# Optimization experiments

Measured on AMD Instinct MI355X. Metric: run time of the kernel, lower is better.

Reference implementation:

```python
import jax, jax.numpy as jnp
import numpy as np
from itertools import permutations
from math import factorial

N_MODES = 6
BATCH = 32768

# Clements mesh mode pairs for 6 modes: alternating odd/even layers, 15 MZIs total.
def clements_mode_list(n=6):
    pairs = []
    for layer in range(n):
        start = 0 if layer % 2 == 0 else 1
        for m in range(start, n - 1, 2):
            pairs.append((m, m + 1))
    return pairs

CLEMENTS_MODES = clements_mode_list(6)            # 15 pairs
ANSATZ_MODES = [(0, 1), (2, 3), (4, 5), (1, 2), (3, 4)] * 2  # 10 pairs (0-indexed)

IN_CONFIG = [1, 1, 1, 0, 0, 0]
OUT_CONFIGS = [list(c) for c in [
    [1,1,1,0,0,0],[1,1,0,1,0,0],[1,1,0,0,1,0],[1,1,0,0,0,1],[1,0,1,1,0,0],
    [1,0,1,0,1,0],[1,0,1,0,0,1],[1,0,0,1,1,0],[1,0,0,1,0,1],[1,0,0,0,1,1],
    [0,1,1,1,0,0],[0,1,1,0,1,0],[0,1,1,0,0,1],[0,1,0,1,1,0],[0,1,0,1,0,1],
    [0,1,0,0,1,1],[0,0,1,1,1,0],[0,0,1,1,0,1],[0,0,1,0,1,1],[0,0,0,1,1,1]]]

def _expand(config):  # occupation list -> repeated mode indices
    idx = []
    for m, c in enumerate(config):
        idx += [m] * int(c)
    return idx

IN_IDX = np.array(_expand(IN_CONFIG))                       # [3]
OUT_IDX = np.array([_expand(c) for c in OUT_CONFIGS])       # [20, 3]
N_PH = IN_IDX.shape[0]                                      # 3 photons
PERMS = list(permutations(range(N_PH)))                     # 6 perms of S_3
# boson-sampling normalization: sqrt(prod(in!) * prod(out!)) per output config (all 1 here)
NORM = np.array([np.sqrt(np.prod([factorial(int(v)) for v in IN_CONFIG]) *
                         np.prod([factorial(int(v)) for v in c])) for c in OUT_CONFIGS],
                dtype=np.float32)


def calc_unitary(modes, theta, phi):
    """Chain of MZI 2x2 rotations embedded in a 6x6 identity (Clements convention)."""
    U = jnp.eye(N_MODES, dtype=jnp.complex64)
    for k, (m, n) in enumerate(modes):
        ct = jnp.cos(theta[k]).astype(jnp.complex64)
        st = jnp.sin(theta[k]).astype(jnp.complex64)
        ep = jnp.exp(1j * phi[k].astype(jnp.complex64))
        T = jnp.eye(N_MODES, dtype=jnp.complex64)
        T = T.at[m, m].set(ep * ct).at[m, n].set(-st)
        T = T.at[n, m].set(ep * st).at[n, n].set(ct)
        U = T @ U
    return U


def permanent3(M):  # M: [..., 3, 3] complex -> [...] permanent over S_3
    acc = jnp.zeros(M.shape[:-2], dtype=M.dtype)
    for p in PERMS:
        acc = acc + M[..., 0, p[0]] * M[..., 1, p[1]] * M[..., 2, p[2]]
    return acc


def setup_inputs() -> dict:
    key = jax.random.key(0)
    ks = jax.random.split(key, 7)
    return {
        "x": jax.random.normal(ks[0], (BATCH, 12), dtype=jnp.float32),
        "params": jax.random.normal(ks[1], (30,), dtype=jnp.float32),
        "output_phase": jax.random.normal(ks[2], (6,), dtype=jnp.float32),
        "param_phi": jax.random.normal(ks[3], (4,), dtype=jnp.float32),
        "param_theta": jax.random.normal(ks[4], (4,), dtype=jnp.float32),
        "input_k": jax.random.normal(ks[5], (12,), dtype=jnp.float32),
        "input_b": jax.random.normal(ks[6], (12,), dtype=jnp.float32),
    }


def reference(x, params, output_phase, param_phi, param_theta, input_k, input_b):
    B = x.shape[0]
    # Static 6x6 interferometer: phi = params[0:15], theta = params[15:30]
    start = calc_unitary(CLEMENTS_MODES, params[15:30], params[0:15])
    start = jnp.diag(jnp.exp(1j * output_phase.astype(jnp.complex64))) @ start

    # Data-reuploading ansatz angles, [B, 10] each
    xs = x * input_k + input_b
    phi = jnp.concatenate([xs[:, 0:3], jnp.broadcast_to(param_phi[0:2], (B, 2)),
                           xs[:, 6:9], jnp.broadcast_to(param_phi[2:4], (B, 2))], axis=1)
    theta = jnp.concatenate([xs[:, 3:6], jnp.broadcast_to(param_theta[0:2], (B, 2)),
                             xs[:, 9:12], jnp.broadcast_to(param_theta[2:4], (B, 2))], axis=1)

    U_ans = jax.vmap(lambda t, p: calc_unitary(ANSATZ_MODES, t, p))(theta, phi)  # [B,6,6]
    U_final = U_ans @ start                                                      # [B,6,6]

    # Boson-sampling amplitudes: permanent of [out rows, in cols] submatrix
    sub = U_final[:, OUT_IDX[:, :, None], IN_IDX[None, None, :]]  # [B, 20, 3, 3]
    amps = permanent3(sub) / jnp.asarray(NORM)                    # [B, 20] complex

    # F.normalize(p=2, dim=1, eps=1e-12) on complex vectors
    norm = jnp.sqrt(jnp.sum(jnp.abs(amps) ** 2, axis=1, keepdims=True))
    amps = amps / jnp.maximum(norm, 1e-12)
    return jnp.abs(amps)
```

## Files before the change

### kernel.cpp

```cpp
#include <hip/hip_runtime.h>
#include <math.h>


__global__ __launch_bounds__(64) void bqnn_kernel(
    const float* __restrict__ x,
    const float* __restrict__ params,
    const float* __restrict__ output_phase,
    const float* __restrict__ param_phi,
    const float* __restrict__ param_theta,
    const float* __restrict__ input_k,
    const float* __restrict__ input_b,
    float* __restrict__ out,
    int B)
{
    __shared__ float sc[88];
    int lane = threadIdx.x;
    int b = blockIdx.x * 64 + lane;
    int bl = (b < B) ? b : (B - 1);

    const float4* xp = reinterpret_cast<const float4*>(x + (size_t)bl * 12);
    float4 a0 = xp[0], a1 = xp[1], a2 = xp[2];

    if (lane < 44) {
        float arg;
        if      (lane < 15) arg = params[15 + lane];
        else if (lane < 30) arg = params[lane - 15];
        else if (lane < 36) arg = output_phase[lane - 30];
        else if (lane < 40) arg = param_theta[lane - 36];
        else                arg = param_phi[lane - 40];
        float s, c;
        __sincosf(arg, &s, &c);
        sc[2 * lane]     = s;
        sc[2 * lane + 1] = c;
    }
    __syncthreads();

    const int CM[15][2] = {{0,1},{2,3},{4,5},{1,2},{3,4},
                           {0,1},{2,3},{4,5},{1,2},{3,4},
                           {0,1},{2,3},{4,5},{1,2},{3,4}};
    float Vre[6][3], Vim[6][3];
    #pragma unroll
    for (int r = 0; r < 6; ++r)
        #pragma unroll
        for (int c = 0; c < 3; ++c) { Vre[r][c] = (r == c) ? 1.f : 0.f; Vim[r][c] = 0.f; }
    #pragma unroll
    for (int k = 0; k < 15; ++k) {
        float pst = sc[2 * k],        pct = sc[2 * k + 1];
        float pei = sc[2 * (15 + k)], per = sc[2 * (15 + k) + 1];
        int m = CM[k][0], n = CM[k][1];
        #pragma unroll
        for (int c = 0; c < 3; ++c) {
            float ar = Vre[m][c], ai = Vim[m][c];
            float br = Vre[n][c], bi = Vim[n][c];
            float tr = per * ar - pei * ai;
            float ti = per * ai + pei * ar;
            Vre[m][c] = pct * tr - pst * br;
            Vim[m][c] = pct * ti - pst * bi;
            Vre[n][c] = pst * tr + pct * br;
            Vim[n][c] = pst * ti + pct * bi;
        }
    }
    #pragma unroll
    for (int r = 0; r < 6; ++r) {
        float pi = sc[2 * (30 + r)], pr = sc[2 * (30 + r) + 1];
        #pragma unroll
        for (int c = 0; c < 3; ++c) {
            float vr = Vre[r][c], vi = Vim[r][c];
            Vre[r][c] = pr * vr - pi * vi;
            Vim[r][c] = pr * vi + pi * vr;
        }
    }

    float xs[12] = {a0.x, a0.y, a0.z, a0.w, a1.x, a1.y, a1.z, a1.w, a2.x, a2.y, a2.z, a2.w};
    #pragma unroll
    for (int i = 0; i < 12; ++i) xs[i] = xs[i] * input_k[i] + input_b[i];

    float ct[10], st[10], epr[10], epi[10];
    __sincosf(xs[3],  &st[0], &ct[0]);  __sincosf(xs[0], &epi[0], &epr[0]);
    __sincosf(xs[4],  &st[1], &ct[1]);  __sincosf(xs[1], &epi[1], &epr[1]);
    __sincosf(xs[5],  &st[2], &ct[2]);  __sincosf(xs[2], &epi[2], &epr[2]);
    st[3] = sc[2*36]; ct[3] = sc[2*36+1];  epi[3] = sc[2*40]; epr[3] = sc[2*40+1];
    st[4] = sc[2*37]; ct[4] = sc[2*37+1];  epi[4] = sc[2*41]; epr[4] = sc[2*41+1];
    __sincosf(xs[9],  &st[5], &ct[5]);  __sincosf(xs[6], &epi[5], &epr[5]);
    __sincosf(xs[10], &st[6], &ct[6]);  __sincosf(xs[7], &epi[6], &epr[6]);
    __sincosf(xs[11], &st[7], &ct[7]);  __sincosf(xs[8], &epi[7], &epr[7]);
    st[8] = sc[2*38]; ct[8] = sc[2*38+1];  epi[8] = sc[2*42]; epr[8] = sc[2*42+1];
    st[9] = sc[2*39]; ct[9] = sc[2*39+1];  epi[9] = sc[2*43]; epr[9] = sc[2*43+1];

    const int AM[10][2] = {{0,1},{2,3},{4,5},{1,2},{3,4},{0,1},{2,3},{4,5},{1,2},{3,4}};
    #pragma unroll
    for (int k = 0; k < 10; ++k) {
        int m = AM[k][0], n = AM[k][1];
        #pragma unroll
        for (int c = 0; c < 3; ++c) {
            float ar = Vre[m][c], ai = Vim[m][c];
            float br = Vre[n][c], bi = Vim[n][c];
            float tr = epr[k] * ar - epi[k] * ai;
            float ti = epr[k] * ai + epi[k] * ar;
            Vre[m][c] = ct[k] * tr - st[k] * br;
            Vim[m][c] = ct[k] * ti - st[k] * bi;
            Vre[n][c] = st[k] * tr + ct[k] * br;
            Vim[n][c] = st[k] * ti + ct[k] * bi;
        }
    }

    const int PR[10][2] = {{1,2},{1,3},{1,4},{1,5},{2,3},{2,4},{2,5},{3,4},{3,5},{4,5}};
    float q01r[10], q01i[10], q02r[10], q02i[10], q12r[10], q12i[10];
    #pragma unroll
    for (int p = 0; p < 10; ++p) {
        int i = PR[p][0], j = PR[p][1];
        q01r[p] = (Vre[i][0]*Vre[j][1] - Vim[i][0]*Vim[j][1]) + (Vre[i][1]*Vre[j][0] - Vim[i][1]*Vim[j][0]);
        q01i[p] = (Vre[i][0]*Vim[j][1] + Vim[i][0]*Vre[j][1]) + (Vre[i][1]*Vim[j][0] + Vim[i][1]*Vre[j][0]);
        q02r[p] = (Vre[i][0]*Vre[j][2] - Vim[i][0]*Vim[j][2]) + (Vre[i][2]*Vre[j][0] - Vim[i][2]*Vim[j][0]);
        q02i[p] = (Vre[i][0]*Vim[j][2] + Vim[i][0]*Vre[j][2]) + (Vre[i][2]*Vim[j][0] + Vim[i][2]*Vre[j][0]);
        q12r[p] = (Vre[i][1]*Vre[j][2] - Vim[i][1]*Vim[j][2]) + (Vre[i][2]*Vre[j][1] - Vim[i][2]*Vim[j][1]);
        q12i[p] = (Vre[i][1]*Vim[j][2] + Vim[i][1]*Vre[j][2]) + (Vre[i][2]*Vim[j][1] + Vim[i][2]*Vre[j][1]);
    }

    const int TA[20] = {0,0,0,0,0,0,0,0,0,0, 1,1,1,1,1,1, 2,2,2, 3};
    const int TP[20] = {0,1,2,3,4,5,6,7,8,9, 4,5,6,7,8,9, 7,8,9, 9};
    float sq[20];
    float ssum = 0.f;
    #pragma unroll
    for (int t = 0; t < 20; ++t) {
        int a = TA[t], p = TP[t];
        float pr = (Vre[a][0]*q12r[p] - Vim[a][0]*q12i[p])
                 + (Vre[a][1]*q02r[p] - Vim[a][1]*q02i[p])
                 + (Vre[a][2]*q01r[p] - Vim[a][2]*q01i[p]);
        float pi = (Vre[a][0]*q12i[p] + Vim[a][0]*q12r[p])
                 + (Vre[a][1]*q02i[p] + Vim[a][1]*q02r[p])
                 + (Vre[a][2]*q01i[p] + Vim[a][2]*q01r[p]);
        sq[t] = pr * pr + pi * pi;
        ssum += sq[t];
    }
    float inv = rsqrtf(fmaxf(ssum, 1e-24f));

    if (b < B) {
        float res[20];
        #pragma unroll
        for (int t = 0; t < 20; ++t) res[t] = sqrtf(sq[t]) * inv;
        float4* op = reinterpret_cast<float4*>(out + (size_t)b * 20);
        op[0] = make_float4(res[0],  res[1],  res[2],  res[3]);
        op[1] = make_float4(res[4],  res[5],  res[6],  res[7]);
        op[2] = make_float4(res[8],  res[9],  res[10], res[11]);
        op[3] = make_float4(res[12], res[13], res[14], res[15]);
        op[4] = make_float4(res[16], res[17], res[18], res[19]);
    }
}

extern "C" void kernel_launch(void* const* d_in, const int* in_sizes, int n_in,
                              void* d_out, int out_size, void* d_ws, size_t ws_size,
                              hipStream_t stream) {
    const float* x            = (const float*)d_in[0];
    const float* params       = (const float*)d_in[1];
    const float* output_phase = (const float*)d_in[2];
    const float* param_phi    = (const float*)d_in[3];
    const float* param_theta  = (const float*)d_in[4];
    const float* input_k      = (const float*)d_in[5];
    const float* input_b      = (const float*)d_in[6];
    int B = in_sizes[0] / 12;

    int block = 64;
    int grid = (B + block - 1) / block;
    bqnn_kernel<<<grid, block, 0, stream>>>(x, params, output_phase, param_phi,
                                            param_theta, input_k, input_b,
                                            (float*)d_out, B);
}
```

Measured before the change: 11.99 us.

## Split each batch element across two threads and parallelize static mesh via shuffles

Each batch element is now handled by two threads. Each thread computes 10 of the 20 permanents, using a row-reversed view of the unitary so that the second half reuses the same code, and the two halves combine their norms with a lane shuffle. The sample-independent Clements mesh is computed once per block, with 18 lanes each holding one matrix entry and exchanging values through shuffles, then broadcast through shared memory. This doubles the thread count and duplicates the x loads, sincos calls and ansatz work per element, in exchange for halving the permanent work per thread and removing the serial 15-MZI chain from every thread.

After: 10.89 us. -9.2%, faster.

```diff
diff --git a/kernel.cpp b/kernel.cpp
--- a/kernel.cpp
+++ b/kernel.cpp
@@ -14,62 +14,95 @@
     int B)
 {
     __shared__ float sc[88];
-    int lane = threadIdx.x;
-    int b = blockIdx.x * 64 + lane;
-    int bl = (b < B) ? b : (B - 1);
-
-    const float4* xp = reinterpret_cast<const float4*>(x + (size_t)bl * 12);
+    __shared__ float sS[36];
+
+    int l = threadIdx.x;
+    long long tid = (long long)blockIdx.x * 64 + l;
+    int e   = (int)(tid >> 1);
+    int sub = (int)(tid & 1);
+    int el  = (e < B) ? e : (B - 1);
+
+    const float4* xp = reinterpret_cast<const float4*>(x + (size_t)el * 12);
     float4 a0 = xp[0], a1 = xp[1], a2 = xp[2];
 
-    if (lane < 44) {
+    if (l < 44) {
         float arg;
-        if      (lane < 15) arg = params[15 + lane];
-        else if (lane < 30) arg = params[lane - 15];
-        else if (lane < 36) arg = output_phase[lane - 30];
-        else if (lane < 40) arg = param_theta[lane - 36];
-        else                arg = param_phi[lane - 40];
+        if      (l < 15) arg = params[15 + l];
+        else if (l < 30) arg = params[l - 15];
+        else if (l < 36) arg = output_phase[l - 30];
+        else if (l < 40) arg = param_theta[l - 36];
+        else             arg = param_phi[l - 40];
         float s, c;
         __sincosf(arg, &s, &c);
-        sc[2 * lane]     = s;
-        sc[2 * lane + 1] = c;
+        sc[2 * l]     = s;
+        sc[2 * l + 1] = c;
     }
     __syncthreads();
 
-    const int CM[15][2] = {{0,1},{2,3},{4,5},{1,2},{3,4},
-                           {0,1},{2,3},{4,5},{1,2},{3,4},
-                           {0,1},{2,3},{4,5},{1,2},{3,4}};
-    float Vre[6][3], Vim[6][3];
+    int ls = (l < 18) ? l : 0;
+    int r_ = ls / 3, c_ = ls - 3 * r_;
+    bool upperA = ((r_ & 1) == 0);
+    int  pA = (r_ ^ 1) * 3 + c_;
+    int  mB = (r_ == 1) ? 2 : (r_ == 2) ? 1 : (r_ == 3) ? 4 : (r_ == 4) ? 3 : r_;
+    int  pB = mB * 3 + c_;
+    bool activeB = (r_ >= 1 && r_ <= 4);
+    bool upperB  = (r_ == 1) || (r_ == 3);
+    int  kA = r_ >> 1;
+    int  kB = (r_ >= 3) ? 1 : 0;
+
+    float ur = (r_ == c_) ? 1.f : 0.f;
+    float ui = 0.f;
+
+    #pragma unroll
+    for (int g = 0; g < 3; ++g) {
+        {
+            int kk = 5 * g + kA;
+            float pst = sc[2 * kk],        pct = sc[2 * kk + 1];
+            float pei = sc[2 * (15 + kk)], per = sc[2 * (15 + kk) + 1];
+            float wr = __shfl(ur, pA, 64), wi = __shfl(ui, pA, 64);
+            float srr = upperA ? ur : wr,  sii = upperA ? ui : wi;
+            float orr = upperA ? wr : ur,  oii = upperA ? wi : ui;
+            float tr = per * srr - pei * sii;
+            float ti = per * sii + pei * srr;
+            float cA = upperA ? pct : pst;
+            float cB = upperA ? -pst : pct;
+            ur = cA * tr + cB * orr;
+            ui = cA * ti + cB * oii;
+        }
+        {
+            int kk = 5 * g + 3 + kB;
+            float pst = sc[2 * kk],        pct = sc[2 * kk + 1];
+            float pei = sc[2 * (15 + kk)], per = sc[2 * (15 + kk) + 1];
+            float wr = __shfl(ur, pB, 64), wi = __shfl(ui, pB, 64);
+            float srr = upperB ? ur : wr,  sii = upperB ? ui : wi;
+            float orr = upperB ? wr : ur,  oii = upperB ? wi : ui;
+            float tr = per * srr - pei * sii;
+            float ti = per * sii + pei * srr;
+            float cA = upperB ? pct : pst;
+            float cB = upperB ? -pst : pct;
+            float nr = cA * tr + cB * orr;
+            float ni = cA * ti + cB * oii;
+            ur = activeB ? nr : ur;
+            ui = activeB ? ni : ui;
+        }
+    }
+    {
+        float opi = sc[2 * (30 + r_)], opr_ = sc[2 * (30 + r_) + 1];
+        float nr = opr_ * ur - opi * ui;
+        float ni = opr_ * ui + opi * ur;
+        ur = nr; ui = ni;
+    }
+    if (l < 18) { sS[2 * l] = ur; sS[2 * l + 1] = ui; }
+    __syncthreads();
+
+    float Sre[6][3], Sim[6][3];
     #pragma unroll
     for (int r = 0; r < 6; ++r)
         #pragma unroll
-        for (int c = 0; c < 3; ++c) { Vre[r][c] = (r == c) ? 1.f : 0.f; Vim[r][c] = 0.f; }
-    #pragma unroll
-    for (int k = 0; k < 15; ++k) {
-        float pst = sc[2 * k],        pct = sc[2 * k + 1];
-        float pei = sc[2 * (15 + k)], per = sc[2 * (15 + k) + 1];
-        int m = CM[k][0], n = CM[k][1];
-        #pragma unroll
         for (int c = 0; c < 3; ++c) {
-            float ar = Vre[m][c], ai = Vim[m][c];
-            float br = Vre[n][c], bi = Vim[n][c];
-            float tr = per * ar - pei * ai;
-            float ti = per * ai + pei * ar;
-            Vre[m][c] = pct * tr - pst * br;
-            Vim[m][c] = pct * ti - pst * bi;
-            Vre[n][c] = pst * tr + pct * br;
-            Vim[n][c] = pst * ti + pct * bi;
-        }
-    }
-    #pragma unroll
-    for (int r = 0; r < 6; ++r) {
-        float pi = sc[2 * (30 + r)], pr = sc[2 * (30 + r) + 1];
-        #pragma unroll
-        for (int c = 0; c < 3; ++c) {
-            float vr = Vre[r][c], vi = Vim[r][c];
-            Vre[r][c] = pr * vr - pi * vi;
-            Vim[r][c] = pr * vi + pi * vr;
-        }
-    }
+            Sre[r][c] = sS[2 * (r * 3 + c)];
+            Sim[r][c] = sS[2 * (r * 3 + c) + 1];
+        }
 
     float xs[12] = {a0.x, a0.y, a0.z, a0.w, a1.x, a1.y, a1.z, a1.w, a2.x, a2.y, a2.z, a2.w};
     #pragma unroll
@@ -87,6 +120,12 @@
     st[8] = sc[2*38]; ct[8] = sc[2*38+1];  epi[8] = sc[2*42]; epr[8] = sc[2*42+1];
     st[9] = sc[2*39]; ct[9] = sc[2*39+1];  epi[9] = sc[2*43]; epr[9] = sc[2*43+1];
 
+    float Vre[6][3], Vim[6][3];
+    #pragma unroll
+    for (int r = 0; r < 6; ++r)
+        #pragma unroll
+        for (int c = 0; c < 3; ++c) { Vre[r][c] = Sre[r][c]; Vim[r][c] = Sim[r][c]; }
+
     const int AM[10][2] = {{0,1},{2,3},{4,5},{1,2},{3,4},{0,1},{2,3},{4,5},{1,2},{3,4}};
     #pragma unroll
     for (int k = 0; k < 10; ++k) {
@@ -104,47 +143,62 @@
         }
     }
 
-    const int PR[10][2] = {{1,2},{1,3},{1,4},{1,5},{2,3},{2,4},{2,5},{3,4},{3,5},{4,5}};
-    float q01r[10], q01i[10], q02r[10], q02i[10], q12r[10], q12i[10];
-    #pragma unroll
-    for (int p = 0; p < 10; ++p) {
-        int i = PR[p][0], j = PR[p][1];
-        q01r[p] = (Vre[i][0]*Vre[j][1] - Vim[i][0]*Vim[j][1]) + (Vre[i][1]*Vre[j][0] - Vim[i][1]*Vim[j][0]);
-        q01i[p] = (Vre[i][0]*Vim[j][1] + Vim[i][0]*Vre[j][1]) + (Vre[i][1]*Vim[j][0] + Vim[i][1]*Vre[j][0]);
-        q02r[p] = (Vre[i][0]*Vre[j][2] - Vim[i][0]*Vim[j][2]) + (Vre[i][2]*Vre[j][0] - Vim[i][2]*Vim[j][0]);
-        q02i[p] = (Vre[i][0]*Vim[j][2] + Vim[i][0]*Vre[j][2]) + (Vre[i][2]*Vim[j][0] + Vim[i][2]*Vre[j][0]);
-        q12r[p] = (Vre[i][1]*Vre[j][2] - Vim[i][1]*Vim[j][2]) + (Vre[i][2]*Vre[j][1] - Vim[i][2]*Vim[j][1]);
-        q12i[p] = (Vre[i][1]*Vim[j][2] + Vim[i][1]*Vre[j][2]) + (Vre[i][2]*Vim[j][1] + Vim[i][2]*Vre[j][1]);
-    }
-
-    const int TA[20] = {0,0,0,0,0,0,0,0,0,0, 1,1,1,1,1,1, 2,2,2, 3};
-    const int TP[20] = {0,1,2,3,4,5,6,7,8,9, 4,5,6,7,8,9, 7,8,9, 9};
-    float sq[20];
+    float Ure[6][3], Uim[6][3];
+    #pragma unroll
+    for (int r = 0; r < 6; ++r)
+        #pragma unroll
+        for (int c = 0; c < 3; ++c) {
+            Ure[r][c] = sub ? Vre[5 - r][c] : Vre[r][c];
+            Uim[r][c] = sub ? Vim[5 - r][c] : Vim[r][c];
+        }
+
+    const int PR2[8][2] = {{1,2},{1,3},{1,4},{1,5},{2,3},{2,4},{2,5},{3,4}};
+    float q01r[8], q01i[8], q02r[8], q02i[8], q12r[8], q12i[8];
+    #pragma unroll
+    for (int p = 0; p < 8; ++p) {
+        int i = PR2[p][0], j = PR2[p][1];
+        q01r[p] = (Ure[i][0]*Ure[j][1] - Uim[i][0]*Uim[j][1]) + (Ure[i][1]*Ure[j][0] - Uim[i][1]*Uim[j][0]);
+        q01i[p] = (Ure[i][0]*Uim[j][1] + Uim[i][0]*Ure[j][1]) + (Ure[i][1]*Uim[j][0] + Uim[i][1]*Ure[j][0]);
+        q02r[p] = (Ure[i][0]*Ure[j][2] - Uim[i][0]*Uim[j][2]) + (Ure[i][2]*Ure[j][0] - Uim[i][2]*Uim[j][0]);
+        q02i[p] = (Ure[i][0]*Uim[j][2] + Uim[i][0]*Ure[j][2]) + (Ure[i][2]*Uim[j][0] + Uim[i][2]*Ure[j][0]);
+        q12r[p] = (Ure[i][1]*Ure[j][2] - Uim[i][1]*Uim[j][2]) + (Ure[i][2]*Ure[j][1] - Uim[i][2]*Uim[j][1]);
+        q12i[p] = (Ure[i][1]*Uim[j][2] + Uim[i][1]*Ure[j][2]) + (Ure[i][2]*Uim[j][1] + Uim[i][2]*Ure[j][1]);
+    }
+
+    const int TA2[10] = {0,0,0,0,0,0,0,0,1,1};
+    const int TQ2[10] = {0,1,2,3,4,5,6,7,4,5};
+    float sq[10];
     float ssum = 0.f;
     #pragma unroll
-    for (int t = 0; t < 20; ++t) {
-        int a = TA[t], p = TP[t];
-        float pr = (Vre[a][0]*q12r[p] - Vim[a][0]*q12i[p])
-                 + (Vre[a][1]*q02r[p] - Vim[a][1]*q02i[p])
-                 + (Vre[a][2]*q01r[p] - Vim[a][2]*q01i[p]);
-        float pi = (Vre[a][0]*q12i[p] + Vim[a][0]*q12r[p])
-                 + (Vre[a][1]*q02i[p] + Vim[a][1]*q02r[p])
-                 + (Vre[a][2]*q01i[p] + Vim[a][2]*q01r[p]);
+    for (int t = 0; t < 10; ++t) {
+        int a = TA2[t], p = TQ2[t];
+        float pr = (Ure[a][0]*q12r[p] - Uim[a][0]*q12i[p])
+                 + (Ure[a][1]*q02r[p] - Uim[a][1]*q02i[p])
+                 + (Ure[a][2]*q01r[p] - Uim[a][2]*q01i[p]);
+        float pi = (Ure[a][0]*q12i[p] + Uim[a][0]*q12r[p])
+                 + (Ure[a][1]*q02i[p] + Uim[a][1]*q02r[p])
+                 + (Ure[a][2]*q01i[p] + Uim[a][2]*q01r[p]);
         sq[t] = pr * pr + pi * pi;
         ssum += sq[t];
     }
+
+    ssum += __shfl_xor(ssum, 1, 64);
     float inv = rsqrtf(fmaxf(ssum, 1e-24f));
 
-    if (b < B) {
-        float res[20];
-        #pragma unroll
-        for (int t = 0; t < 20; ++t) res[t] = sqrtf(sq[t]) * inv;
-        float4* op = reinterpret_cast<float4*>(out + (size_t)b * 20);
-        op[0] = make_float4(res[0],  res[1],  res[2],  res[3]);
-        op[1] = make_float4(res[4],  res[5],  res[6],  res[7]);
-        op[2] = make_float4(res[8],  res[9],  res[10], res[11]);
-        op[3] = make_float4(res[12], res[13], res[14], res[15]);
-        op[4] = make_float4(res[16], res[17], res[18], res[19]);
+    if (e < B) {
+        float o[10];
+        #pragma unroll
+        for (int t = 0; t < 10; ++t) o[t] = sqrtf(sq[t]) * inv;
+        float* base = out + (size_t)e * 20;
+        if (sub == 0) {
+            *reinterpret_cast<float4*>(base + 0)  = make_float4(o[0], o[1], o[2], o[3]);
+            *reinterpret_cast<float4*>(base + 4)  = make_float4(o[4], o[5], o[6], o[7]);
+            *reinterpret_cast<float2*>(base + 10) = make_float2(o[8], o[9]);
+        } else {
+            *reinterpret_cast<float2*>(base + 8)  = make_float2(o[6], o[3]);
+            *reinterpret_cast<float4*>(base + 12) = make_float4(o[7], o[9], o[5], o[2]);
+            *reinterpret_cast<float4*>(base + 16) = make_float4(o[8], o[4], o[1], o[0]);
+        }
     }
 }
 
@@ -160,8 +214,9 @@
     const float* input_b      = (const float*)d_in[6];
     int B = in_sizes[0] / 12;
 
+    long long threads = (long long)B * 2;
     int block = 64;
-    int grid = (B + block - 1) / block;
+    int grid = (int)((threads + block - 1) / block);
     bqnn_kernel<<<grid, block, 0, stream>>>(x, params, output_phase, param_phi,
                                             param_theta, input_k, input_b,
                                             (float*)d_out, B);
```
